# Kernel optimization log

Hardware: AMD Instinct MI355X
Metric: run time of the kernel (lower is better)

The kernel has to match this reference:

```python
import jax, jax.numpy as jnp
import numpy as np

RADIUS = 0.1
NSAMPLE = 32
STRIDE = 4
EPS = 1e-5


def fps(p, M):
    # Furthest point sampling. p: [B, N, 3] -> idx [B, M] int32. First point is index 0.
    B, N, _ = p.shape

    def body(carry, _):
        dmin, last = carry
        lp = jnp.take_along_axis(p, last[:, None, None], axis=1)  # [B,1,3]
        d = jnp.sum((p - lp) ** 2, axis=-1)                       # [B,N]
        dmin = jnp.minimum(dmin, d)
        nxt = jnp.argmax(dmin, axis=-1).astype(jnp.int32)
        return (dmin, nxt), nxt

    first = jnp.zeros((B,), jnp.int32)
    dmin0 = jnp.full((B, N), jnp.inf, p.dtype)
    _, rest = jax.lax.scan(body, (dmin0, first), None, length=M - 1)
    return jnp.concatenate([first[None, :], rest], axis=0).T  # [B,M]


def ball_query(new_p, p, radius, K):
    # For each query, first K support indices with dist < radius (CUDA ballquery semantics:
    # pad with first found index; 0 if none). new_p [B,M,3], p [B,N,3] -> [B,M,K] int32.
    N = p.shape[1]
    d2 = (jnp.sum(new_p ** 2, -1)[:, :, None] + jnp.sum(p ** 2, -1)[:, None, :]
          - 2.0 * jnp.einsum('bmd,bnd->bmn', new_p, p))  # [B,M,N]
    scores = jnp.where(d2 < radius * radius,
                       jnp.arange(N, dtype=jnp.int32)[None, None, :], N)
    neg_vals, _ = jax.lax.top_k(-scores, K)  # K smallest scores, ascending
    idx = -neg_vals
    first = jnp.where(idx[..., :1] >= N, 0, idx[..., :1])
    return jnp.where(idx >= N, first, idx)


def bn(x, g, b):
    # BatchNorm (training-mode batch stats) over all dims except channel dim 1.
    axes = tuple(i for i in range(x.ndim) if i != 1)
    m = jnp.mean(x, axes, keepdims=True)
    v = jnp.var(x, axes, keepdims=True)
    shape = (1, -1) + (1,) * (x.ndim - 2)
    return g.reshape(shape) * (x - m) * jax.lax.rsqrt(v + EPS) + b.reshape(shape)


def setup_inputs() -> dict:
    key = jax.random.key(0)
    ks = jax.random.split(key, 6)
    B, N, C = 4, 8192, 64
    return {
        'p': jax.random.uniform(ks[0], (B, N, 3), jnp.float32),
        'f': jax.random.normal(ks[1], (B, C, N), jnp.float32),
        'w1': jax.random.normal(ks[2], (64, 3 + C), jnp.float32) * 0.05,
        'g1': jnp.ones((64,), jnp.float32),
        'b1': jnp.zeros((64,), jnp.float32),
        'w2': jax.random.normal(ks[3], (128, 64), jnp.float32) * 0.05,
        'g2': jnp.ones((128,), jnp.float32),
        'b2': jnp.zeros((128,), jnp.float32),
        'w_skip': jax.random.normal(ks[4], (128, C), jnp.float32) * 0.05,
        'b_skip': jnp.zeros((128,), jnp.float32),
    }


def reference(p, f, w1, g1, b1, w2, g2, b2, w_skip, b_skip):
    B, N, _ = p.shape
    C = f.shape[1]
    M = N // STRIDE
    idx = fps(p, M)                                                # [B,M]
    new_p = jnp.take_along_axis(p, idx[:, :, None], axis=1)        # [B,M,3]
    # residual branch: gather sampled features, 1x1 conv1d skip
    fi = jnp.take_along_axis(f, jnp.broadcast_to(idx[:, None, :], (B, C, M)), axis=2)
    identity = jnp.einsum('oc,bcm->bom', w_skip, fi) + b_skip[None, :, None]
    # ball-query grouping
    nidx = ball_query(new_p, p, RADIUS, NSAMPLE)                   # [B,M,K]
    flat = nidx.reshape(B, 1, M * NSAMPLE)
    pj = jnp.take_along_axis(p.transpose(0, 2, 1),
                             jnp.broadcast_to(flat, (B, 3, M * NSAMPLE)),
                             axis=2).reshape(B, 3, M, NSAMPLE)
    dp = pj - new_p.transpose(0, 2, 1)[:, :, :, None]              # [B,3,M,K]
    fj = jnp.take_along_axis(f, jnp.broadcast_to(flat, (B, C, M * NSAMPLE)),
                             axis=2).reshape(B, C, M, NSAMPLE)
    x = jnp.concatenate([dp, fj], axis=1)                          # [B,3+C,M,K]
    # conv-bn-relu, conv-bn (last block no act because use_res)
    x = jax.nn.relu(bn(jnp.einsum('oc,bcmk->bomk', w1, x), g1, b1))
    x = bn(jnp.einsum('oc,bcmk->bomk', w2, x), g2, b2)
    fout = jnp.max(x, axis=-1)                                     # [B,128,M]
    fout = jax.nn.relu(fout + identity)
    return new_p, fout, idx
```

## Files before the change

kernel.cpp:

```cpp
#include <hip/hip_runtime.h>
#include <math.h>

#define BB 4
#define NP 8192
#define CF 64
#define MQ 2048
#define KS 32

#define WS_FT     0u
#define WS_NIDX   2097152u
#define WS_IDXI   2359296u
#define WS_ST1    2367488u
#define WS_ST2    2375680u
#define WS_SC1    2392064u
#define WS_SC2    2392192u
#define WS_MAXY2  2392448u
#define WS_W1P    3441024u

typedef float v2f __attribute__((ext_vector_type(2)));
typedef unsigned long long u64;

__global__ __launch_bounds__(256) void transpose_f_kernel(
    const float* __restrict__ f, float* __restrict__ ft) {
  __shared__ float tile[64][65];
  int b = blockIdx.y;
  int n0 = blockIdx.x * 64;
  int cc = threadIdx.x >> 6;
  int nn = threadIdx.x & 63;
  #pragma unroll
  for (int r = 0; r < 16; ++r) {
    int c = cc * 16 + r;
    tile[c][nn] = f[((size_t)b * 64 + c) * NP + n0 + nn];
  }
  __syncthreads();
  #pragma unroll
  for (int r = 0; r < 16; ++r) {
    int nl = cc * 16 + r;
    ft[((size_t)b * NP + n0 + nl) * 64 + nn] = tile[nn][nl];
  }
}

__global__ void prep_w1_kernel(const float* __restrict__ w1, float* __restrict__ w1p) {
  int i = blockIdx.x * 256 + threadIdx.x;
  if (i < 64 * 68) {
    int o = i / 68, c = i % 68;
    w1p[i] = (c < 67) ? w1[o * 67 + c] : 0.0f;
  }
}

#define FPS_T 512
#define SLOTS 16

template <int CTRL>
__device__ __forceinline__ u64 dpp_max_step(u64 k) {
  int lo = (int)(unsigned)k;
  int hi = (int)(unsigned)(k >> 32);
  int slo = __builtin_amdgcn_update_dpp(0, lo, CTRL, 0xF, 0xF, true);
  int shi = __builtin_amdgcn_update_dpp(0, hi, CTRL, 0xF, 0xF, true);
  u64 s = ((u64)(unsigned)shi << 32) | (u64)(unsigned)slo;
  return s > k ? s : k;
}

__global__ __launch_bounds__(512, 1) void fps_kernel(
    const float* __restrict__ p, float* __restrict__ out, int* __restrict__ idx_i) {
#pragma clang fp contract(off)
  __shared__ float4 sp4[NP];
  __shared__ int win[MQ];
  __shared__ u64 cnd[3];
  int b = blockIdx.x;
  const float* pb = p + (size_t)b * NP * 3;
  float* out_newp = out;
  float* out_idxf = out + BB*MQ*3 + (size_t)BB*128*MQ;
  int t = threadIdx.x;
  int lane = t & 63;
  int wv = t >> 6;

  float tx[SLOTS], ty[SLOTS], tz[SLOTS];
  int cells[SLOTS];
  win[t] = 0;
  __syncthreads();
  #pragma unroll
  for (int s = 0; s < SLOTS; ++s) {
    int i = s * FPS_T + t;
    float x = pb[i*3+0], y = pb[i*3+1], z = pb[i*3+2];
    tx[s] = x; ty[s] = y; tz[s] = z;
    int cx = (int)(x * 8.0f); cx = cx < 0 ? 0 : (cx > 7 ? 7 : cx);
    int cy = (int)(y * 8.0f); cy = cy < 0 ? 0 : (cy > 7 ? 7 : cy);
    int cz = (int)(z * 8.0f); cz = cz < 0 ? 0 : (cz > 7 ? 7 : cz);
    int mx = (cx & 1) | ((cx & 2) << 2) | ((cx & 4) << 4);
    int my = (cy & 1) | ((cy & 2) << 2) | ((cy & 4) << 4);
    int mz = (cz & 1) | ((cz & 2) << 2) | ((cz & 4) << 4);
    int cell = mx | (my << 1) | (mz << 2);
    cells[s] = cell;
    atomicAdd(&win[cell], 1);
  }
  __syncthreads();
  {
    int myCnt = win[t];
    int* sA = win; int* sB = win + 512;
    __syncthreads();
    bool a2b = true;
    for (int off = 1; off < 512; off <<= 1) {
      int* src = a2b ? sA : sB; int* dst = a2b ? sB : sA;
      int v = src[t];
      if (t >= off) v += src[t - off];
      dst[t] = v;
      a2b = !a2b;
      __syncthreads();
    }
    int incl = sB[t];
    __syncthreads();
    win[t] = incl - myCnt;
  }
  __syncthreads();
  for (int w = 0; w < 8; ++w) {
    if (wv == w) {
      #pragma unroll
      for (int s = 0; s < SLOTS; ++s) {
        int c = cells[s];
        u64 eq = ~0ull;
        #pragma unroll
        for (int bit = 0; bit < 9; ++bit) {
          u64 bset = __ballot(((c >> bit) & 1) != 0);
          eq &= (((c >> bit) & 1) ? bset : ~bset);
        }
        int rank = (int)__popcll(eq & ((1ull << lane) - 1ull));
        int leader = (int)__builtin_ctzll(eq);
        int base = 0;
        if (lane == leader) base = atomicAdd(&win[c], (int)__popcll(eq));
        base = __shfl(base, leader);
        sp4[base + rank] = make_float4(tx[s], ty[s], tz[s],
                                       __int_as_float(s * FPS_T + t));
      }
    }
    __syncthreads();
  }
  unsigned notI[SLOTS];
  float bminx = INFINITY, bminy = INFINITY, bminz = INFINITY;
  float bmaxx = -INFINITY, bmaxy = -INFINITY, bmaxz = -INFINITY;
  #pragma unroll
  for (int s = 0; s < SLOTS; ++s) {
    float4 q = sp4[t * SLOTS + s];
    tx[s] = q.x; ty[s] = q.y; tz[s] = q.z;
    notI[s] = ~(unsigned)__float_as_int(q.w);
    bminx = fminf(bminx, q.x); bmaxx = fmaxf(bmaxx, q.x);
    bminy = fminf(bminy, q.y); bmaxy = fmaxf(bmaxy, q.y);
    bminz = fminf(bminz, q.z); bmaxz = fmaxf(bmaxz, q.z);
  }
  __syncthreads();
  #pragma unroll
  for (int s = 0; s < SLOTS; ++s) {
    int oi = (int)(~notI[s]);
    sp4[oi] = make_float4(tx[s], ty[s], tz[s], 0.0f);
  }
  if (t < 3) cnd[t] = 0ull;
  if (t == 0) win[0] = 0;
  v2f px2[8], py2[8], pz2[8], dmin2[8];
  #pragma unroll
  for (int k = 0; k < 8; ++k) {
    px2[k] = (v2f){tx[2*k], tx[2*k+1]};
    py2[k] = (v2f){ty[2*k], ty[2*k+1]};
    pz2[k] = (v2f){tz[2*k], tz[2*k+1]};
    dmin2[k] = (v2f){INFINITY, INFINITY};
  }
  __syncthreads();
  float lx = sp4[0].x, ly = sp4[0].y, lz = sp4[0].z;

  float bvCache = INFINITY;
  u64 cachedKey = 0ull;
  for (int j = 1; j < MQ; ++j) {
    float dxm = fmaxf(fmaxf(bminx - lx, lx - bmaxx), 0.0f);
    float dym = fmaxf(fmaxf(bminy - ly, ly - bmaxy), 0.0f);
    float dzm = fmaxf(fmaxf(bminz - lz, lz - bmaxz), 0.0f);
    float lbsq = dxm*dxm + dym*dym + dzm*dzm;
    if (!(lbsq * 0.999f >= bvCache)) {
      v2f l2x = (v2f){lx, lx}, l2y = (v2f){ly, ly}, l2z = (v2f){lz, lz};
      u64 c0 = 0ull, c1 = 0ull;
      #pragma unroll
      for (int k = 0; k < 8; ++k) {
        v2f dx = px2[k] - l2x;
        v2f dy = py2[k] - l2y;
        v2f dz = pz2[k] - l2z;
        v2f dd = ((dx*dx) + (dy*dy)) + (dz*dz);
        v2f dm = __builtin_elementwise_min(dmin2[k], dd);
        dmin2[k] = dm;
        u64 k0 = ((u64)__float_as_uint(dm.x) << 32) | (u64)notI[2*k];
        u64 k1 = ((u64)__float_as_uint(dm.y) << 32) | (u64)notI[2*k+1];
        c0 = k0 > c0 ? k0 : c0;
        c1 = k1 > c1 ? k1 : c1;
      }
      cachedKey = c0 > c1 ? c0 : c1;
      bvCache = __uint_as_float((unsigned)(cachedKey >> 32));
    }
    u64 key = cachedKey;
    key = dpp_max_step<0x111>(key);
    key = dpp_max_step<0x112>(key);
    key = dpp_max_step<0x114>(key);
    key = dpp_max_step<0x118>(key);
    key = dpp_max_step<0x142>(key);
    key = dpp_max_step<0x143>(key);
    int slot = j % 3;
    if (lane == 63) atomicMax(&cnd[slot], key);
    __syncthreads();
    u64 kw = cnd[slot];
    if (t == 0) cnd[(j + 2) % 3] = 0ull;
    int wi = (int)(~(unsigned)kw);
    float4 c = sp4[wi];
    lx = c.x; ly = c.y; lz = c.z;
    if (t == 0) win[j] = wi;
  }

  __syncthreads();
  #pragma unroll
  for (int k2 = 0; k2 < MQ / FPS_T; ++k2) {
    int j = k2 * FPS_T + t;
    int wi = win[j];
    out_idxf[b*MQ + j] = (float)wi;
    idx_i[b*MQ + j] = wi;
    float4 c = sp4[wi];
    float* np_ = &out_newp[(size_t)(b*MQ + j) * 3];
    np_[0] = c.x; np_[1] = c.y; np_[2] = c.z;
  }
}

__global__ __launch_bounds__(256) void ballq_kernel(
    const float* __restrict__ p, const float* __restrict__ newp,
    int* __restrict__ nidx) {
  int qid = blockIdx.x * 4 + (threadIdx.x >> 6);
  int lane = threadIdx.x & 63;
  int b = qid >> 11;
  const float* pb = p + (size_t)b * NP * 3;
  float qx = newp[qid*3], qy = newp[qid*3+1], qz = newp[qid*3+2];
  float sq_q = __fadd_rn(__fadd_rn(__fmul_rn(qx,qx), __fmul_rn(qy,qy)), __fmul_rn(qz,qz));
  const float R2 = (float)(0.1 * 0.1);
  int found = 0, first = -1;
  int* outp = nidx + (size_t)qid * KS;
  for (int base = 0; base < NP; base += 64) {
    int n = base + lane;
    float x = pb[n*3], y = pb[n*3+1], z = pb[n*3+2];
    float sq_p = __fadd_rn(__fadd_rn(__fmul_rn(x,x), __fmul_rn(y,y)), __fmul_rn(z,z));
    float dot  = __fadd_rn(__fadd_rn(__fmul_rn(qx,x), __fmul_rn(qy,y)), __fmul_rn(qz,z));
    float d2   = __fadd_rn(__fadd_rn(sq_q, sq_p), __fmul_rn(-2.0f, dot));
    bool hit = d2 < R2;
    unsigned long long mask = __ballot(hit);
    if (mask) {
      if (first < 0) first = base + __builtin_ctzll(mask);
      int cnt = __popcll(mask);
      if (found < KS) {
        int rank = __popcll(mask & ((1ull << lane) - 1ull));
        if (hit && found + rank < KS) outp[found + rank] = n;
      }
      found += cnt;
      if (found >= KS) break;
    }
  }
  int fcl = found < KS ? found : KS;
  int padv = first < 0 ? 0 : first;
  if (lane >= fcl && lane < KS) outp[lane] = padv;
}

__global__ __launch_bounds__(256) void p1_kernel(
    const float* __restrict__ p, const float* __restrict__ newp,
    const float* __restrict__ ft, const int* __restrict__ nidx,
    const float* __restrict__ w1p, float* __restrict__ stats1) {
  __shared__ __align__(16) float xbuf[4][KS][68];
  __shared__ float wbs[4][64], wbq[4][64];
  int wv = threadIdx.x >> 6, lane = threadIdx.x & 63;
  int qid = blockIdx.x * 4 + wv;
  int b = qid >> 11;
  int nv = (lane < KS) ? nidx[(size_t)qid * KS + lane] : 0;
  float qx = newp[qid*3], qy = newp[qid*3+1], qz = newp[qid*3+2];
  for (int kk = 0; kk < KS; ++kk) {
    int n = __shfl(nv, kk);
    const float* fr = ft + ((size_t)b * NP + n) * 64;
    xbuf[wv][kk][3 + lane] = fr[lane];
    if (lane < 3) {
      const float* pp = p + ((size_t)b * NP + n) * 3;
      float qc = (lane == 0) ? qx : ((lane == 1) ? qy : qz);
      xbuf[wv][kk][lane] = __fsub_rn(pp[lane], qc);
    }
    if (lane == 3) xbuf[wv][kk][67] = 0.0f;
  }
  __syncthreads();
  const float4* wr = (const float4*)(w1p + lane * 68);
  float4 wreg[17];
  #pragma unroll
  for (int c4 = 0; c4 < 17; ++c4) wreg[c4] = wr[c4];
  float ss = 0.f, qq = 0.f;
  for (int kk = 0; kk < KS; ++kk) {
    const float4* xr = (const float4*)(&xbuf[wv][kk][0]);
    float acc = 0.f;
    #pragma unroll
    for (int c4 = 0; c4 < 17; ++c4) {
      float4 w = wreg[c4]; float4 x = xr[c4];
      acc += w.x*x.x + w.y*x.y + w.z*x.z + w.w*x.w;
    }
    ss += acc; qq += acc * acc;
  }
  wbs[wv][lane] = ss; wbq[wv][lane] = qq;
  __syncthreads();
  if (threadIdx.x < 64) {
    float s  = wbs[0][threadIdx.x] + wbs[1][threadIdx.x] + wbs[2][threadIdx.x] + wbs[3][threadIdx.x];
    float s2 = wbq[0][threadIdx.x] + wbq[1][threadIdx.x] + wbq[2][threadIdx.x] + wbq[3][threadIdx.x];
    int slice = blockIdx.x & 63;
    atomicAdd(&stats1[(slice*2+0)*64 + threadIdx.x], s);
    atomicAdd(&stats1[(slice*2+1)*64 + threadIdx.x], s2);
  }
}

__global__ void fin1_kernel(const float* __restrict__ stats1,
                            const float* __restrict__ g, const float* __restrict__ bb,
                            float* __restrict__ sc) {
  int o = threadIdx.x;
  float s = 0.f, q = 0.f;
  for (int sl = 0; sl < 64; ++sl) { s += stats1[(sl*2+0)*64+o]; q += stats1[(sl*2+1)*64+o]; }
  const float cnt = (float)(BB * MQ * KS);
  float mean = s / cnt;
  float var = q / cnt - mean * mean;
  float rstd = 1.0f / sqrtf(var + 1e-5f);
  float gs = g[o] * rstd;
  sc[o] = gs;
  sc[64+o] = bb[o] - mean * gs;
}

__global__ void fin2_kernel(const float* __restrict__ stats2,
                            const float* __restrict__ g, const float* __restrict__ bb,
                            float* __restrict__ sc) {
  int o = threadIdx.x;
  float s = 0.f, q = 0.f;
  for (int sl = 0; sl < 64; ++sl) { s += stats2[(sl*2+0)*128+o]; q += stats2[(sl*2+1)*128+o]; }
  const float cnt = (float)(BB * MQ * KS);
  float mean = s / cnt;
  float var = q / cnt - mean * mean;
  float rstd = 1.0f / sqrtf(var + 1e-5f);
  float gs = g[o] * rstd;
  sc[o] = gs;
  sc[128+o] = bb[o] - mean * gs;
}

__global__ __launch_bounds__(256) void p2_kernel(
    const float* __restrict__ p, const float* __restrict__ newp,
    const float* __restrict__ ft, const int* __restrict__ nidx,
    const float* __restrict__ w1p, const float* __restrict__ w2,
    const float* __restrict__ sc1,
    float* __restrict__ stats2, float* __restrict__ maxy2) {
  __shared__ __align__(16) float xbuf[4][KS][68];
  __shared__ float wbs[4][128], wbq[4][128];
  int wv = threadIdx.x >> 6, lane = threadIdx.x & 63;
  int qid = blockIdx.x * 4 + wv;
  int b = qid >> 11;
  int nv = (lane < KS) ? nidx[(size_t)qid * KS + lane] : 0;
  float qx = newp[qid*3], qy = newp[qid*3+1], qz = newp[qid*3+2];
  for (int kk = 0; kk < KS; ++kk) {
    int n = __shfl(nv, kk);
    const float* fr = ft + ((size_t)b * NP + n) * 64;
    xbuf[wv][kk][3 + lane] = fr[lane];
    if (lane < 3) {
      const float* pp = p + ((size_t)b * NP + n) * 3;
      float qc = (lane == 0) ? qx : ((lane == 1) ? qy : qz);
      xbuf[wv][kk][lane] = __fsub_rn(pp[lane], qc);
    }
    if (lane == 3) xbuf[wv][kk][67] = 0.0f;
  }
  __syncthreads();
  {
    const float4* wr = (const float4*)(w1p + lane * 68);
    float4 wreg[17];
    #pragma unroll
    for (int c4 = 0; c4 < 17; ++c4) wreg[c4] = wr[c4];
    float s1v = sc1[lane], t1v = sc1[64 + lane];
    for (int kk = 0; kk < KS; ++kk) {
      const float4* xr = (const float4*)(&xbuf[wv][kk][0]);
      float acc = 0.f;
      #pragma unroll
      for (int c4 = 0; c4 < 17; ++c4) {
        float4 w = wreg[c4]; float4 x = xr[c4];
        acc += w.x*x.x + w.y*x.y + w.z*x.z + w.w*x.w;
      }
      float h = fmaxf(0.0f, fmaf(acc, s1v, t1v));
      xbuf[wv][kk][lane] = h;
    }
  }
  const float4* w2a = (const float4*)(w2 + (size_t)lane * 64);
  const float4* w2b = (const float4*)(w2 + (size_t)(lane + 64) * 64);
  float4 wra[16], wrb[16];
  #pragma unroll
  for (int c4 = 0; c4 < 16; ++c4) { wra[c4] = w2a[c4]; wrb[c4] = w2b[c4]; }
  float ss0 = 0.f, qq0 = 0.f, mx0 = -INFINITY;
  float ss1 = 0.f, qq1 = 0.f, mx1 = -INFINITY;
  for (int kk = 0; kk < KS; ++kk) {
    const float4* hr = (const float4*)(&xbuf[wv][kk][0]);
    float a0 = 0.f, a1 = 0.f;
    #pragma unroll
    for (int c4 = 0; c4 < 16; ++c4) {
      float4 h4 = hr[c4];
      float4 wa = wra[c4]; float4 wb = wrb[c4];
      a0 += wa.x*h4.x + wa.y*h4.y + wa.z*h4.z + wa.w*h4.w;
      a1 += wb.x*h4.x + wb.y*h4.y + wb.z*h4.z + wb.w*h4.w;
    }
    ss0 += a0; qq0 += a0*a0; mx0 = fmaxf(mx0, a0);
    ss1 += a1; qq1 += a1*a1; mx1 = fmaxf(mx1, a1);
  }
  maxy2[(size_t)qid * 128 + lane] = mx0;
  maxy2[(size_t)qid * 128 + 64 + lane] = mx1;
  wbs[wv][lane] = ss0; wbs[wv][64+lane] = ss1;
  wbq[wv][lane] = qq0; wbq[wv][64+lane] = qq1;
  __syncthreads();
  if (threadIdx.x < 128) {
    float s  = wbs[0][threadIdx.x] + wbs[1][threadIdx.x] + wbs[2][threadIdx.x] + wbs[3][threadIdx.x];
    float s2 = wbq[0][threadIdx.x] + wbq[1][threadIdx.x] + wbq[2][threadIdx.x] + wbq[3][threadIdx.x];
    int slice = blockIdx.x & 63;
    atomicAdd(&stats2[(slice*2+0)*128 + threadIdx.x], s);
    atomicAdd(&stats2[(slice*2+1)*128 + threadIdx.x], s2);
  }
}

__global__ __launch_bounds__(256) void p3_kernel(
    const float* __restrict__ ft, const int* __restrict__ idx_i,
    const float* __restrict__ w_skip, const float* __restrict__ b_skip,
    const float* __restrict__ sc2, const float* __restrict__ maxy2,
    float* __restrict__ outf) {
  int wv = threadIdx.x >> 6, lane = threadIdx.x & 63;
  int qid = blockIdx.x * 4 + wv;
  int b = qid >> 11, m = qid & (MQ - 1);
  int n = idx_i[qid];
  const float4* f4 = (const float4*)(ft + ((size_t)b * NP + n) * 64);
  const float4* wa = (const float4*)(w_skip + (size_t)lane * 64);
  const float4* wb = (const float4*)(w_skip + (size_t)(lane + 64) * 64);
  float a0 = b_skip[lane], a1 = b_skip[lane + 64];
  #pragma unroll
  for (int c4 = 0; c4 < 16; ++c4) {
    float4 x = f4[c4]; float4 u = wa[c4]; float4 v = wb[c4];
    a0 += u.x*x.x + u.y*x.y + u.z*x.z + u.w*x.w;
    a1 += v.x*x.x + v.y*x.y + v.z*x.z + v.w*x.w;
  }
  float v0 = maxy2[(size_t)qid * 128 + lane];
  float v1 = maxy2[(size_t)qid * 128 + 64 + lane];
  float r0 = fmaxf(0.0f, fmaf(v0, sc2[lane],      sc2[128 + lane])      + a0);
  float r1 = fmaxf(0.0f, fmaf(v1, sc2[lane + 64], sc2[128 + lane + 64]) + a1);
  outf[((size_t)b * 128 + lane) * MQ + m] = r0;
  outf[((size_t)b * 128 + lane + 64) * MQ + m] = r1;
}

extern "C" void kernel_launch(void* const* d_in, const int* in_sizes, int n_in,
                              void* d_out, int out_size, void* d_ws, size_t ws_size,
                              hipStream_t stream) {
  (void)in_sizes; (void)n_in; (void)out_size; (void)ws_size;
  const float* p   = (const float*)d_in[0];
  const float* f   = (const float*)d_in[1];
  const float* w1  = (const float*)d_in[2];
  const float* g1  = (const float*)d_in[3];
  const float* b1  = (const float*)d_in[4];
  const float* w2  = (const float*)d_in[5];
  const float* g2  = (const float*)d_in[6];
  const float* b2  = (const float*)d_in[7];
  const float* wsk = (const float*)d_in[8];
  const float* bsk = (const float*)d_in[9];
  float* out = (float*)d_out;
  float* wsf = (float*)d_ws;

  float* ft    = wsf + WS_FT;
  int*   nidx  = (int*)(wsf + WS_NIDX);
  int*   idxi  = (int*)(wsf + WS_IDXI);
  float* st1   = wsf + WS_ST1;
  float* st2   = wsf + WS_ST2;
  float* sc1   = wsf + WS_SC1;
  float* sc2   = wsf + WS_SC2;
  float* maxy2 = wsf + WS_MAXY2;
  float* w1p   = wsf + WS_W1P;

  float* out_newp = out;
  float* out_f    = out + BB*MQ*3;

  (void)hipMemsetAsync(st1, 0, (8192 + 16384) * sizeof(float), stream);

  transpose_f_kernel<<<dim3(NP/64, BB), 256, 0, stream>>>(f, ft);
  prep_w1_kernel<<<17, 256, 0, stream>>>(w1, w1p);
  fps_kernel<<<BB, FPS_T, 0, stream>>>(p, out, idxi);
  ballq_kernel<<<BB*MQ/4, 256, 0, stream>>>(p, out_newp, nidx);
  p1_kernel<<<BB*MQ/4, 256, 0, stream>>>(p, out_newp, ft, nidx, w1p, st1);
  fin1_kernel<<<1, 64, 0, stream>>>(st1, g1, b1, sc1);
  p2_kernel<<<BB*MQ/4, 256, 0, stream>>>(p, out_newp, ft, nidx, w1p, w2, sc1, st2, maxy2);
  fin2_kernel<<<1, 128, 0, stream>>>(st2, g2, b2, sc2);
  p3_kernel<<<BB*MQ/4, 256, 0, stream>>>(ft, idxi, wsk, bsk, sc2, maxy2, out_f);
}
```

Before: 2.209 ms.

## Restructure FPS with 256 threads and per-wave group bounding-box culling

FPS now runs with 256 threads holding 32 points each. Points are re-binned on a coarser z grid and laid out so each wave owns 16 spatial groups of 128 points. Each group keeps its bounding box and max min-distance in shared memory, and a group's distance update is skipped when its box lower bound cannot beat that max. The aim is to prune more per-point distance work per iteration and to make the block-wide barrier and atomic reduction cheaper with fewer waves. In exchange each iteration does more DPP reductions and shared-memory traffic, and per-thread register pressure goes up.

After: 3.330 ms. 50.8% more time.

```diff
diff --git a/kernel.cpp b/kernel.cpp
--- a/kernel.cpp
+++ b/kernel.cpp
@@ -48,8 +48,8 @@
   }
 }
 
-#define FPS_T 512
-#define SLOTS 16
+#define FPS_T 256
+#define SLOTS 32
 
 template <int CTRL>
 __device__ __forceinline__ u64 dpp_max_step(u64 k) {
@@ -60,13 +60,43 @@
   u64 s = ((u64)(unsigned)shi << 32) | (u64)(unsigned)slo;
   return s > k ? s : k;
 }
-
-__global__ __launch_bounds__(512, 1) void fps_kernel(
+__device__ __forceinline__ u64 dpp_max_all(u64 k) {
+  k = dpp_max_step<0x111>(k); k = dpp_max_step<0x112>(k);
+  k = dpp_max_step<0x114>(k); k = dpp_max_step<0x118>(k);
+  k = dpp_max_step<0x142>(k); k = dpp_max_step<0x143>(k);
+  return k;
+}
+template <int CTRL>
+__device__ __forceinline__ float dpp_fmax_step(float x) {
+  int s = __builtin_amdgcn_update_dpp(0, __float_as_int(x), CTRL, 0xF, 0xF, true);
+  return fmaxf(__int_as_float(s), x);
+}
+__device__ __forceinline__ float dpp_fmax_all(float x) {
+  x = dpp_fmax_step<0x111>(x); x = dpp_fmax_step<0x112>(x);
+  x = dpp_fmax_step<0x114>(x); x = dpp_fmax_step<0x118>(x);
+  x = dpp_fmax_step<0x142>(x); x = dpp_fmax_step<0x143>(x);
+  return x;
+}
+template <int CTRL>
+__device__ __forceinline__ float dpp_fmin_step(float x) {
+  int s = __builtin_amdgcn_update_dpp(0x7F800000, __float_as_int(x), CTRL, 0xF, 0xF, false);
+  return fminf(__int_as_float(s), x);
+}
+__device__ __forceinline__ float dpp_fmin_all(float x) {
+  x = dpp_fmin_step<0x111>(x); x = dpp_fmin_step<0x112>(x);
+  x = dpp_fmin_step<0x114>(x); x = dpp_fmin_step<0x118>(x);
+  x = dpp_fmin_step<0x142>(x); x = dpp_fmin_step<0x143>(x);
+  return x;
+}
+
+__global__ __launch_bounds__(256, 1) void fps_kernel(
     const float* __restrict__ p, float* __restrict__ out, int* __restrict__ idx_i) {
 #pragma clang fp contract(off)
   __shared__ float4 sp4[NP];
   __shared__ int win[MQ];
   __shared__ u64 cnd[3];
+  __shared__ float gbox[4][16][8];
+  __shared__ float gbv[4][16];
   int b = blockIdx.x;
   const float* pb = p + (size_t)b * NP * 3;
   float* out_newp = out;
@@ -86,41 +116,38 @@
     tx[s] = x; ty[s] = y; tz[s] = z;
     int cx = (int)(x * 8.0f); cx = cx < 0 ? 0 : (cx > 7 ? 7 : cx);
     int cy = (int)(y * 8.0f); cy = cy < 0 ? 0 : (cy > 7 ? 7 : cy);
-    int cz = (int)(z * 8.0f); cz = cz < 0 ? 0 : (cz > 7 ? 7 : cz);
-    int mx = (cx & 1) | ((cx & 2) << 2) | ((cx & 4) << 4);
-    int my = (cy & 1) | ((cy & 2) << 2) | ((cy & 4) << 4);
-    int mz = (cz & 1) | ((cz & 2) << 2) | ((cz & 4) << 4);
-    int cell = mx | (my << 1) | (mz << 2);
+    int cz = (int)(z * 4.0f); cz = cz < 0 ? 0 : (cz > 3 ? 3 : cz);
+    int cell = (cx & 1) | ((cy & 1) << 1) | ((cz & 1) << 2)
+             | (((cx >> 1) & 1) << 3) | (((cy >> 1) & 1) << 4) | ((cz >> 1) << 5)
+             | ((cx >> 2) << 6) | ((cy >> 2) << 7);
     cells[s] = cell;
     atomicAdd(&win[cell], 1);
   }
   __syncthreads();
   {
     int myCnt = win[t];
-    int* sA = win; int* sB = win + 512;
     __syncthreads();
-    bool a2b = true;
-    for (int off = 1; off < 512; off <<= 1) {
-      int* src = a2b ? sA : sB; int* dst = a2b ? sB : sA;
+    int* src = win; int* dst = win + 256;
+    for (int off = 1; off < 256; off <<= 1) {
       int v = src[t];
       if (t >= off) v += src[t - off];
       dst[t] = v;
-      a2b = !a2b;
+      int* tmp = src; src = dst; dst = tmp;
       __syncthreads();
     }
-    int incl = sB[t];
+    int incl = src[t];
     __syncthreads();
     win[t] = incl - myCnt;
   }
   __syncthreads();
-  for (int w = 0; w < 8; ++w) {
+  for (int w = 0; w < 4; ++w) {
     if (wv == w) {
       #pragma unroll
       for (int s = 0; s < SLOTS; ++s) {
         int c = cells[s];
         u64 eq = ~0ull;
         #pragma unroll
-        for (int bit = 0; bit < 9; ++bit) {
+        for (int bit = 0; bit < 8; ++bit) {
           u64 bset = __ballot(((c >> bit) & 1) != 0);
           eq &= (((c >> bit) & 1) ? bset : ~bset);
         }
@@ -136,16 +163,12 @@
     __syncthreads();
   }
   unsigned notI[SLOTS];
-  float bminx = INFINITY, bminy = INFINITY, bminz = INFINITY;
-  float bmaxx = -INFINITY, bmaxy = -INFINITY, bmaxz = -INFINITY;
   #pragma unroll
   for (int s = 0; s < SLOTS; ++s) {
-    float4 q = sp4[t * SLOTS + s];
-    tx[s] = q.x; ty[s] = q.y; tz[s] = q.z;
-    notI[s] = ~(unsigned)__float_as_int(q.w);
-    bminx = fminf(bminx, q.x); bmaxx = fmaxf(bmaxx, q.x);
-    bminy = fminf(bminy, q.y); bmaxy = fmaxf(bmaxy, q.y);
-    bminz = fminf(bminz, q.z); bmaxz = fmaxf(bmaxz, q.z);
+    int q = wv * 2048 + s * 64 + lane;
+    float4 v = sp4[q];
+    tx[s] = v.x; ty[s] = v.y; tz[s] = v.z;
+    notI[s] = ~(unsigned)__float_as_int(v.w);
   }
   __syncthreads();
   #pragma unroll
@@ -153,54 +176,71 @@
     int oi = (int)(~notI[s]);
     sp4[oi] = make_float4(tx[s], ty[s], tz[s], 0.0f);
   }
-  if (t < 3) cnd[t] = 0ull;
-  if (t == 0) win[0] = 0;
-  v2f px2[8], py2[8], pz2[8], dmin2[8];
-  #pragma unroll
-  for (int k = 0; k < 8; ++k) {
+  v2f px2[16], py2[16], pz2[16], dmin2[16];
+  #pragma unroll
+  for (int k = 0; k < 16; ++k) {
     px2[k] = (v2f){tx[2*k], tx[2*k+1]};
     py2[k] = (v2f){ty[2*k], ty[2*k+1]};
     pz2[k] = (v2f){tz[2*k], tz[2*k+1]};
     dmin2[k] = (v2f){INFINITY, INFINITY};
-  }
-  __syncthreads();
+    float mnx = dpp_fmin_all(fminf(tx[2*k], tx[2*k+1]));
+    float mny = dpp_fmin_all(fminf(ty[2*k], ty[2*k+1]));
+    float mnz = dpp_fmin_all(fminf(tz[2*k], tz[2*k+1]));
+    float mxx = dpp_fmax_all(fmaxf(tx[2*k], tx[2*k+1]));
+    float mxy = dpp_fmax_all(fmaxf(ty[2*k], ty[2*k+1]));
+    float mxz = dpp_fmax_all(fmaxf(tz[2*k], tz[2*k+1]));
+    if (lane == 63) {
+      gbox[wv][k][0] = mnx; gbox[wv][k][1] = mny; gbox[wv][k][2] = mnz;
+      gbox[wv][k][4] = mxx; gbox[wv][k][5] = mxy; gbox[wv][k][6] = mxz;
+      gbv[wv][k] = INFINITY;
+    }
+  }
+  if (t < 3) cnd[t] = 0ull;
+  if (t == 0) win[0] = 0;
+  __syncthreads();
+  int g = lane & 15;
+  float gmnx = gbox[wv][g][0], gmny = gbox[wv][g][1], gmnz = gbox[wv][g][2];
+  float gmxx = gbox[wv][g][4], gmxy = gbox[wv][g][5], gmxz = gbox[wv][g][6];
   float lx = sp4[0].x, ly = sp4[0].y, lz = sp4[0].z;
 
-  float bvCache = INFINITY;
-  u64 cachedKey = 0ull;
+  u64 cachedWaveKey = 0ull;
   for (int j = 1; j < MQ; ++j) {
-    float dxm = fmaxf(fmaxf(bminx - lx, lx - bmaxx), 0.0f);
-    float dym = fmaxf(fmaxf(bminy - ly, ly - bmaxy), 0.0f);
-    float dzm = fmaxf(fmaxf(bminz - lz, lz - bmaxz), 0.0f);
+    float cbv = gbv[wv][g];
+    float dxm = fmaxf(fmaxf(gmnx - lx, lx - gmxx), 0.0f);
+    float dym = fmaxf(fmaxf(gmny - ly, ly - gmxy), 0.0f);
+    float dzm = fmaxf(fmaxf(gmnz - lz, lz - gmxz), 0.0f);
     float lbsq = dxm*dxm + dym*dym + dzm*dzm;
-    if (!(lbsq * 0.999f >= bvCache)) {
+    bool gd = (lbsq * 0.999f < cbv);
+    u64 bm = __ballot(gd);
+    unsigned m16 = (unsigned)(bm & 0xFFFFull);
+    if (m16) {
       v2f l2x = (v2f){lx, lx}, l2y = (v2f){ly, ly}, l2z = (v2f){lz, lz};
+      #pragma unroll
+      for (int k = 0; k < 16; ++k) {
+        if (m16 & (1u << k)) {
+          v2f dx = px2[k] - l2x;
+          v2f dy = py2[k] - l2y;
+          v2f dz = pz2[k] - l2z;
+          v2f dd = ((dx*dx) + (dy*dy)) + (dz*dz);
+          v2f dm = __builtin_elementwise_min(dmin2[k], dd);
+          dmin2[k] = dm;
+          float nb = dpp_fmax_all(fmaxf(dm.x, dm.y));
+          if (lane == 63) gbv[wv][k] = nb;
+        }
+      }
       u64 c0 = 0ull, c1 = 0ull;
       #pragma unroll
-      for (int k = 0; k < 8; ++k) {
-        v2f dx = px2[k] - l2x;
-        v2f dy = py2[k] - l2y;
-        v2f dz = pz2[k] - l2z;
-        v2f dd = ((dx*dx) + (dy*dy)) + (dz*dz);
-        v2f dm = __builtin_elementwise_min(dmin2[k], dd);
-        dmin2[k] = dm;
-        u64 k0 = ((u64)__float_as_uint(dm.x) << 32) | (u64)notI[2*k];
-        u64 k1 = ((u64)__float_as_uint(dm.y) << 32) | (u64)notI[2*k+1];
+      for (int k = 0; k < 16; ++k) {
+        u64 k0 = ((u64)__float_as_uint(dmin2[k].x) << 32) | (u64)notI[2*k];
+        u64 k1 = ((u64)__float_as_uint(dmin2[k].y) << 32) | (u64)notI[2*k+1];
         c0 = k0 > c0 ? k0 : c0;
         c1 = k1 > c1 ? k1 : c1;
       }
-      cachedKey = c0 > c1 ? c0 : c1;
-      bvCache = __uint_as_float((unsigned)(cachedKey >> 32));
-    }
-    u64 key = cachedKey;
-    key = dpp_max_step<0x111>(key);
-    key = dpp_max_step<0x112>(key);
-    key = dpp_max_step<0x114>(key);
-    key = dpp_max_step<0x118>(key);
-    key = dpp_max_step<0x142>(key);
-    key = dpp_max_step<0x143>(key);
+      u64 key = c0 > c1 ? c0 : c1;
+      cachedWaveKey = dpp_max_all(key);
+    }
     int slot = j % 3;
-    if (lane == 63) atomicMax(&cnd[slot], key);
+    if (lane == 63) atomicMax(&cnd[slot], cachedWaveKey);
     __syncthreads();
     u64 kw = cnd[slot];
     if (t == 0) cnd[(j + 2) % 3] = 0ull;
```
